# Performance work log

Measured on AMD Instinct MI355X. Metric: run time of the kernel, lower is better.

Reference implementation:

```python
import jax, jax.numpy as jnp
import numpy as np

N_NODES = 4096
N_EDGES = 32768
IN_FEAT = 256
OUT_FEAT = 128
HID = 64
IN_HEAD = 64
OUT_HEAD = 5
NEG_SLOPE = 0.2
EPS = 1e-16


def setup_inputs() -> dict:
    key = jax.random.key(0)
    ks = jax.random.split(key, 12)
    x = jax.random.normal(ks[0], (N_NODES, IN_FEAT), dtype=jnp.float32)
    src = jax.random.randint(ks[1], (N_EDGES,), 0, N_NODES)
    dst = jax.random.randint(ks[2], (N_EDGES,), 0, N_NODES)
    edge_index = jnp.stack([src, dst]).astype(jnp.int64)
    s1 = 1.0 / np.sqrt(IN_FEAT)
    s2 = 1.0 / np.sqrt(HID * IN_HEAD)
    W1 = jax.random.normal(ks[3], (IN_FEAT, IN_HEAD * HID), dtype=jnp.float32) * s1
    att_src1 = jax.random.normal(ks[4], (IN_HEAD, HID), dtype=jnp.float32) * 0.1
    att_dst1 = jax.random.normal(ks[5], (IN_HEAD, HID), dtype=jnp.float32) * 0.1
    b1 = jnp.zeros((IN_HEAD * HID,), dtype=jnp.float32)
    W2 = jax.random.normal(ks[6], (IN_HEAD * HID, OUT_HEAD * OUT_FEAT), dtype=jnp.float32) * s2
    att_src2 = jax.random.normal(ks[7], (OUT_HEAD, OUT_FEAT), dtype=jnp.float32) * 0.1
    att_dst2 = jax.random.normal(ks[8], (OUT_HEAD, OUT_FEAT), dtype=jnp.float32) * 0.1
    b2 = jnp.zeros((OUT_FEAT,), dtype=jnp.float32)
    return {"x": x, "edge_index": edge_index, "W1": W1, "att_src1": att_src1,
            "att_dst1": att_dst1, "b1": b1, "W2": W2, "att_src2": att_src2,
            "att_dst2": att_dst2, "b2": b2}


def _gat_conv(x, W, att_src, att_dst, bias, src, dst, heads, out_c, concat):
    # x: [N, F_in]; returns [N, heads*out_c] (concat) or [N, out_c] (mean)
    n = x.shape[0]
    h = (x @ W).reshape(n, heads, out_c)                       # [N,H,C]
    a_src = jnp.sum(h * att_src, axis=-1)                      # [N,H]
    a_dst = jnp.sum(h * att_dst, axis=-1)                      # [N,H]
    e = jax.nn.leaky_relu(a_src[src] + a_dst[dst], NEG_SLOPE)  # [E,H]
    # segment softmax over edges grouped by destination node (PyG softmax)
    m = jax.ops.segment_max(e, dst, num_segments=n)            # [N,H]
    ex = jnp.exp(e - m[dst])
    denom = jax.ops.segment_sum(ex, dst, num_segments=n)       # [N,H]
    alpha = ex / (denom[dst] + EPS)                            # [E,H]
    out = jax.ops.segment_sum(alpha[:, :, None] * h[src], dst, num_segments=n)  # [N,H,C]
    out = out.reshape(n, heads * out_c) if concat else out.mean(axis=1)
    return out + bias


def reference(x, edge_index, W1, att_src1, att_dst1, b1, W2, att_src2, att_dst2, b2):
    n = x.shape[0]
    # PyG GATConv default: add self loops
    loop = jnp.arange(n, dtype=edge_index.dtype)
    src = jnp.concatenate([edge_index[0], loop])
    dst = jnp.concatenate([edge_index[1], loop])
    # dropout layers are identity in eval mode
    h = _gat_conv(x, W1, att_src1, att_dst1, b1, src, dst, IN_HEAD, HID, True)
    h = jax.nn.elu(h)
    h = _gat_conv(h, W2, att_src2, att_dst2, b2, src, dst, OUT_HEAD, OUT_FEAT, False)
    s = jnp.mean(h, axis=0)
    return jnp.tanh(s)
```

## Files before the change

kernel.cpp:

```cpp
#include <hip/hip_runtime.h>
#include <hip/hip_bf16.h>

#define N_NODES 4096
#define NE      32768
#define E_TOT   (NE + N_NODES)
#define IN_FEAT 256
#define HID     64
#define IN_HEAD 64
#define F1      4096
#define OUT_HEAD 5
#define OUT_FEAT 128
#define F2      640
#define NEG_SLOPE 0.2f
#define EPS_A   1e-16f

typedef __bf16 bf16;
typedef bf16 bf16x8 __attribute__((ext_vector_type(8)));
typedef bf16 bf16x4 __attribute__((ext_vector_type(4)));
typedef float f32x4 __attribute__((ext_vector_type(4)));

__device__ inline void async_cp16(bf16* lds, const bf16* g) {
    __builtin_amdgcn_global_load_lds(
        (const __attribute__((address_space(1))) unsigned int*)g,
        (__attribute__((address_space(3))) unsigned int*)lds, 16, 0, 0);
}

template <typename TC>
__device__ __forceinline__ void gemm_body(
    const bf16* __restrict__ A, const bf16* __restrict__ BT, TC* __restrict__ Cz,
    int m0, int n0, int kbeg, int kchunk, int Ncols, int Kdim,
    bf16 (*As)[64], bf16 (*Bs)[64], int tid) {
    const int wave = tid >> 6, lane = tid & 63;
    const int quad = lane >> 4, lr = lane & 15;
    const int wm = (wave >> 1) * 64;
    const int wn = (wave & 1) * 64;
    const int srow = lane >> 3;
    const int scol = ((lane & 7) ^ srow) * 8;
    const int xk = lr & 7;

    f32x4 acc[4][4] = {};

    for (int kk = 0; kk < kchunk; kk += 64) {
        int k0 = kbeg + kk;
#pragma unroll
        for (int c = 0; c < 4; ++c) {
            int r = wave * 32 + c * 8;
            async_cp16(&As[r][0], A + (size_t)(m0 + r + srow) * Kdim + k0 + scol);
            async_cp16(&Bs[r][0], BT + (size_t)(n0 + r + srow) * Kdim + k0 + scol);
        }
        __syncthreads();

#pragma unroll
        for (int ks = 0; ks < 2; ++ks) {
            int ch = ((ks * 4 + quad) ^ xk) * 8;
            bf16x8 af[4], bfr[4];
#pragma unroll
            for (int mt = 0; mt < 4; ++mt)
                af[mt] = *(const bf16x8*)(&As[wm + mt * 16 + lr][ch]);
#pragma unroll
            for (int nt = 0; nt < 4; ++nt)
                bfr[nt] = *(const bf16x8*)(&Bs[wn + nt * 16 + lr][ch]);
#pragma unroll
            for (int mt = 0; mt < 4; ++mt)
#pragma unroll
                for (int nt = 0; nt < 4; ++nt)
                    acc[mt][nt] = __builtin_amdgcn_mfma_f32_16x16x32_bf16(
                        af[mt], bfr[nt], acc[mt][nt], 0, 0, 0);
        }
        __syncthreads();
    }

#pragma unroll
    for (int mt = 0; mt < 4; ++mt)
#pragma unroll
        for (int nt = 0; nt < 4; ++nt) {
            int row0 = m0 + wm + mt * 16 + quad * 4;
            int col = n0 + wn + nt * 16 + lr;
#pragma unroll
            for (int r = 0; r < 4; ++r)
                Cz[(size_t)(row0 + r) * Ncols + col] = (TC)acc[mt][nt][r];
        }
}

#define PB_H   144
#define PB_X   512
#define PB_W1  1024
#define PB_W2  2560
__global__ __launch_bounds__(256)
void phaseA_kernel(const int* __restrict__ edst, int* __restrict__ counts,
                   const float* __restrict__ x, bf16* __restrict__ xb,
                   const float* __restrict__ W1, bf16* __restrict__ W1T,
                   const float* __restrict__ W2, bf16* __restrict__ W2T,
                   const float* __restrict__ as1, const float* __restrict__ ad1,
                   bf16* __restrict__ w1s, bf16* __restrict__ w1d) {
    __shared__ float tile[32][33];
    int b0 = blockIdx.x, t = threadIdx.x;
    if (b0 < PB_H) {
        int e = b0 * 256 + t;
        if (e < E_TOT) {
            int d = (e < NE) ? edst[e] : (e - NE);
            atomicAdd(&counts[d], 1);
        }
        return;
    }
    int b = b0 - PB_H;
    if (b < PB_X) {
        int i = b * 256 + t;
        f32x4 a = *(const f32x4*)(x + (size_t)i * 8);
        f32x4 c = *(const f32x4*)(x + (size_t)i * 8 + 4);
        bf16x8 r;
        r[0] = (bf16)a[0]; r[1] = (bf16)a[1]; r[2] = (bf16)a[2]; r[3] = (bf16)a[3];
        r[4] = (bf16)c[0]; r[5] = (bf16)c[1]; r[6] = (bf16)c[2]; r[7] = (bf16)c[3];
        *(bf16x8*)(xb + (size_t)i * 8) = r;
    } else if (b < PB_X + PB_W1 + PB_W2) {
        const float* S; bf16* D; int R, C, gx, gy;
        if (b < PB_X + PB_W1) {
            int bb = b - PB_X;
            S = W1; D = W1T; R = IN_FEAT; C = F1;
            gx = bb % (F1 / 32); gy = bb / (F1 / 32);
        } else {
            int bb = b - PB_X - PB_W1;
            S = W2; D = W2T; R = F1; C = F2;
            gx = bb % (F2 / 32); gy = bb / (F2 / 32);
        }
        int tx = t & 31, ty = t >> 5;
        int c0 = gx * 32, r0 = gy * 32;
#pragma unroll
        for (int i = 0; i < 4; ++i)
            tile[ty + i * 8][tx] = S[(size_t)(r0 + ty + i * 8) * C + c0 + tx];
        __syncthreads();
#pragma unroll
        for (int i = 0; i < 4; ++i)
            D[(size_t)(c0 + ty + i * 8) * R + r0 + tx] = (bf16)tile[tx][ty + i * 8];
    } else {
        int id = (b - PB_X - PB_W1 - PB_W2) * 256 + t;
        int k = id >> 6, h = id & 63;
        const float* wrow = W1 + (size_t)k * F1 + h * HID;
        const float* a1 = as1 + h * HID;
        const float* a2 = ad1 + h * HID;
        float s = 0.f, d = 0.f;
#pragma unroll 8
        for (int c = 0; c < HID; ++c) {
            float w = wrow[c];
            s += w * a1[c];
            d += w * a2[c];
        }
        w1s[id] = (bf16)s;
        w1d[id] = (bf16)d;
    }
}

__global__ void scan_kernel(const int* __restrict__ counts,
                            int* __restrict__ row_start, int* __restrict__ cursor) {
    __shared__ int part[256];
    __shared__ int pre[257];
    int t = threadIdx.x;
    int base = t * 16;
    int local[16];
    int s = 0;
#pragma unroll
    for (int i = 0; i < 16; ++i) { local[i] = s; s += counts[base + i]; }
    part[t] = s;
    __syncthreads();
    if (t == 0) {
        int r = 0;
        for (int i = 0; i < 256; ++i) { pre[i] = r; r += part[i]; }
        pre[256] = r;
    }
    __syncthreads();
    int off = pre[t];
#pragma unroll
    for (int i = 0; i < 16; ++i) {
        int v = off + local[i];
        row_start[base + i] = v;
        cursor[base + i] = v;
    }
    if (t == 0) row_start[N_NODES] = pre[256];
}

#define PC_S   144
#define PC_G1  1024
__global__ __launch_bounds__(256)
void phaseC_kernel(const int* __restrict__ edst, int* cursor, int* __restrict__ elist,
                   const bf16* __restrict__ xb, const bf16* __restrict__ W1T,
                   bf16* __restrict__ H1,
                   const float* __restrict__ x,
                   const bf16* __restrict__ w1s, const bf16* __restrict__ w1d,
                   float* __restrict__ a_src, float* __restrict__ a_dst) {
    __shared__ bf16 As[128][64];
    __shared__ bf16 Bs[128][64];
    int b = blockIdx.x, t = threadIdx.x;
    if (b < PC_S) {
        int e = b * 256 + t;
        if (e < E_TOT) {
            int d = (e < NE) ? edst[e] : (e - NE);
            int slot = atomicAdd(&cursor[d], 1);
            elist[slot] = e;
        }
    } else if (b < PC_S + PC_G1) {
        int bid = b - PC_S;
        int xx = bid & 7, q = bid >> 3;
        int mb = xx * 4 + (q >> 5);
        int nb = q & 31;
        gemm_body<bf16>(xb, W1T, H1, mb * 128, nb * 128, 0, IN_FEAT,
                        F1, IN_FEAT, As, Bs, t);
    } else {
        int nblk = b - PC_S - PC_G1;
        int wave = t >> 6, lane = t & 63;
        int n = nblk * 4 + wave;
        const float* xr = x + (size_t)n * IN_FEAT;
        float s = 0.f, d = 0.f;
        for (int k0 = 0; k0 < IN_FEAT; k0 += 4) {
            f32x4 xv = *(const f32x4*)(xr + k0);
#pragma unroll
            for (int j = 0; j < 4; ++j) {
                float xs = xv[j];
                s += xs * (float)w1s[(k0 + j) * IN_HEAD + lane];
                d += xs * (float)w1d[(k0 + j) * IN_HEAD + lane];
            }
        }
        a_src[n * IN_HEAD + lane] = s;
        a_dst[n * IN_HEAD + lane] = d;
    }
}

__global__ __launch_bounds__(64)
void agg1_kernel(const int* __restrict__ es, const int* __restrict__ row_start,
                 const int* __restrict__ elist,
                 const float* __restrict__ a_src, const float* __restrict__ a_dst,
                 const bf16* __restrict__ H1, const float* __restrict__ b1,
                 bf16* __restrict__ h_elu) {
    int bid = blockIdx.x;
    int c = bid & 7;
    int d = bid >> 3;
    int lane = threadIdx.x;
    int gh = c * 8 + (lane >> 3);
    int sub = lane & 7;
    int beg = row_start[d], deg = row_start[d + 1] - beg;
    float adst = a_dst[d * IN_HEAD + gh];

    float m = -1e30f, den = 0.f;
    for (int i = sub; i < deg; i += 8) {
        int e = elist[beg + i];
        int s = (e < NE) ? es[e] : d;
        float l = a_src[s * IN_HEAD + gh] + adst;
        l = l > 0.f ? l : NEG_SLOPE * l;
        if (l > m) { den = den * __expf(m - l) + 1.f; m = l; }
        else den += __expf(l - m);
    }
#pragma unroll
    for (int o = 1; o <= 4; o <<= 1) {
        float mo = __shfl_xor(m, o);
        float dno = __shfl_xor(den, o);
        float mn = fmaxf(m, mo);
        den = den * __expf(m - mn) + dno * __expf(mo - mn);
        m = mn;
    }
    float dinv = 1.f / (den + EPS_A);

    int fbase = c * 512 + lane * 8;
    float acc[8] = {};
#pragma unroll 2
    for (int i = 0; i < deg; ++i) {
        int e = elist[beg + i];
        int s = (e < NE) ? es[e] : d;
        float l = a_src[s * IN_HEAD + gh] + adst;
        l = l > 0.f ? l : NEG_SLOPE * l;
        float alpha = __expf(l - m) * dinv;
        bf16x8 v = *(const bf16x8*)(H1 + (size_t)s * F1 + fbase);
#pragma unroll
        for (int j = 0; j < 8; ++j) acc[j] += alpha * (float)v[j];
    }

    bf16x8 o;
#pragma unroll
    for (int j = 0; j < 8; ++j) {
        float v = acc[j] + b1[fbase + j];
        o[j] = (bf16)(v > 0.f ? v : (__expf(v) - 1.f));
    }
    *(bf16x8*)(h_elu + (size_t)d * F1 + fbase) = o;
}

__global__ __launch_bounds__(256)
void gemm2_kernel(const bf16* __restrict__ A, const bf16* __restrict__ BT,
                  bf16* __restrict__ C) {
    __shared__ bf16 As[128][64];
    __shared__ bf16 Bs[128][64];
    int bid = blockIdx.x;
    int xx = bid & 7, q = bid >> 3;
    int gp = q / 5, nb = q - gp * 5;
    int g = gp * 8 + xx;
    int mb = g >> 2, zb = g & 3;
    const int kchunk = F1 / 4;
    gemm_body<bf16>(A, BT, C + (size_t)zb * N_NODES * F2,
                    mb * 128, nb * 128, zb * kchunk, kchunk,
                    F2, F1, As, Bs, threadIdx.x);
}

__global__ __launch_bounds__(192)
void fold2_kernel(const bf16* __restrict__ Hp,
                  const float* __restrict__ as2, const float* __restrict__ ad2,
                  float* __restrict__ H2,
                  float* __restrict__ a_src, float* __restrict__ a_dst) {
    int n = blockIdx.x, t = threadIdx.x;
    if (t >= 160) return;
    int h = t >> 5;
    f32x4 sum = {};
#pragma unroll
    for (int z = 0; z < 4; ++z) {
        bf16x4 v = *(const bf16x4*)(Hp + (size_t)z * N_NODES * F2 + (size_t)n * F2 + t * 4);
        sum[0] += (float)v[0]; sum[1] += (float)v[1];
        sum[2] += (float)v[2]; sum[3] += (float)v[3];
    }
    *(f32x4*)(H2 + (size_t)n * F2 + t * 4) = sum;
    f32x4 ws = *(const f32x4*)(as2 + t * 4);
    f32x4 wd = *(const f32x4*)(ad2 + t * 4);
    float s = sum[0] * ws[0] + sum[1] * ws[1] + sum[2] * ws[2] + sum[3] * ws[3];
    float d = sum[0] * wd[0] + sum[1] * wd[1] + sum[2] * wd[2] + sum[3] * wd[3];
#pragma unroll
    for (int o = 1; o <= 16; o <<= 1) {
        s += __shfl_xor(s, o);
        d += __shfl_xor(d, o);
    }
    if ((t & 31) == 0) {
        a_src[n * OUT_HEAD + h] = s;
        a_dst[n * OUT_HEAD + h] = d;
    }
}

__global__ void statsbeta2_kernel(const int* __restrict__ es,
                                  const int* __restrict__ row_start,
                                  const int* __restrict__ elist,
                                  const float* __restrict__ a_src,
                                  const float* __restrict__ a_dst,
                                  float* __restrict__ beta) {
    int id = blockIdx.x * 256 + threadIdx.x;
    if (id >= N_NODES * OUT_HEAD) return;
    int d = id / OUT_HEAD, h = id - d * OUT_HEAD;
    int beg = row_start[d], deg = row_start[d + 1] - beg;
    float adst = a_dst[id];
    float m = -1e30f, den = 0.f;
    for (int i = 0; i < deg; ++i) {
        int e = elist[beg + i];
        int s = (e < NE) ? es[e] : d;
        float l = a_src[s * OUT_HEAD + h] + adst;
        l = l > 0.f ? l : NEG_SLOPE * l;
        if (l > m) { den = den * __expf(m - l) + 1.f; m = l; }
        else den += __expf(l - m);
    }
    float dinv = 1.f / (den + EPS_A);
    for (int i = 0; i < deg; ++i) {
        int e = elist[beg + i];
        int s = (e < NE) ? es[e] : d;
        float l = a_src[s * OUT_HEAD + h] + adst;
        l = l > 0.f ? l : NEG_SLOPE * l;
        float alpha = __expf(l - m) * dinv;
        atomicAdd(&beta[s * OUT_HEAD + h], alpha);
    }
}

__global__ __launch_bounds__(256)
void wsum_kernel(const float* __restrict__ H2, const float* __restrict__ beta,
                 float* __restrict__ acc_out, int* __restrict__ done_ctr,
                 const float* __restrict__ b2, float* __restrict__ out) {
    __shared__ float buf[F2];
    __shared__ int lflag;
    int t = threadIdx.x;
    int n0 = blockIdx.x * 32;
    int h = t >> 5;
    float a0 = 0.f, a1 = 0.f, a2 = 0.f, a3 = 0.f;
    if (t < 160) {
        for (int i = 0; i < 32; ++i) {
            int s = n0 + i;
            float bh = beta[s * OUT_HEAD + h];
            f32x4 v = *(const f32x4*)(H2 + (size_t)s * F2 + t * 4);
            a0 += bh * v[0]; a1 += bh * v[1];
            a2 += bh * v[2]; a3 += bh * v[3];
        }
        buf[t * 4 + 0] = a0; buf[t * 4 + 1] = a1;
        buf[t * 4 + 2] = a2; buf[t * 4 + 3] = a3;
    }
    __syncthreads();
    if (t < OUT_FEAT) {
        float s = 0.f;
#pragma unroll
        for (int hh = 0; hh < OUT_HEAD; ++hh) s += buf[hh * OUT_FEAT + t];
        atomicAdd(&acc_out[(blockIdx.x & 7) * OUT_FEAT + t], s);
    }
    __threadfence();
    __syncthreads();
    if (t == 0) lflag = (atomicAdd(done_ctr, 1) == (N_NODES / 32) - 1);
    __syncthreads();
    if (lflag && t < OUT_FEAT) {
        float tot = 0.f;
#pragma unroll
        for (int k = 0; k < 8; ++k)
            tot += __hip_atomic_load(&acc_out[k * OUT_FEAT + t],
                                     __ATOMIC_RELAXED, __HIP_MEMORY_SCOPE_AGENT);
        out[t] = tanhf(tot * (1.f / (OUT_HEAD * (float)N_NODES)) + b2[t]);
    }
}

extern "C" void kernel_launch(void* const* d_in, const int* in_sizes, int n_in,
                              void* d_out, int out_size, void* d_ws, size_t ws_size,
                              hipStream_t stream) {
    const float* x        = (const float*)d_in[0];
    const int*   ei       = (const int*)d_in[1];
    const float* W1       = (const float*)d_in[2];
    const float* att_src1 = (const float*)d_in[3];
    const float* att_dst1 = (const float*)d_in[4];
    const float* b1       = (const float*)d_in[5];
    const float* W2       = (const float*)d_in[6];
    const float* att_src2 = (const float*)d_in[7];
    const float* att_dst2 = (const float*)d_in[8];
    const float* b2       = (const float*)d_in[9];
    float* out = (float*)d_out;

    const int* esrc = ei;
    const int* edst = ei + NE;

    char* p = (char*)d_ws;
    auto bump = [&](size_t bytes) {
        void* r = (void*)p;
        p += (bytes + 255) & ~(size_t)255;
        return r;
    };
    bf16*  H1     = (bf16*)bump((size_t)N_NODES * F1 * 2);
    bf16*  h_elu  = (bf16*)bump((size_t)N_NODES * F1 * 2);
    float* H2     = (float*)bump((size_t)N_NODES * F2 * 4);
    bf16*  xb     = (bf16*)bump((size_t)N_NODES * IN_FEAT * 2);
    bf16*  W1T    = (bf16*)bump((size_t)F1 * IN_FEAT * 2);
    bf16*  W2T    = (bf16*)bump((size_t)F2 * F1 * 2);
    bf16*  w1s    = (bf16*)bump((size_t)IN_FEAT * IN_HEAD * 2);
    bf16*  w1d    = (bf16*)bump((size_t)IN_FEAT * IN_HEAD * 2);
    float* a_src1 = (float*)bump((size_t)N_NODES * IN_HEAD * 4);
    float* a_dst1 = (float*)bump((size_t)N_NODES * IN_HEAD * 4);
    float* a_src2 = (float*)bump((size_t)N_NODES * OUT_HEAD * 4);
    float* a_dst2 = (float*)bump((size_t)N_NODES * OUT_HEAD * 4);
    int*   row_start = (int*)bump((N_NODES + 1) * 4);
    int*   cursor = (int*)bump(N_NODES * 4);
    int*   elist  = (int*)bump(E_TOT * 4);
    size_t zbytes = N_NODES * 4 + N_NODES * OUT_HEAD * 4 + 8 * OUT_FEAT * 4 + 256;
    int*   counts = (int*)bump(zbytes);
    float* beta    = (float*)((char*)counts + N_NODES * 4);
    float* acc_out = beta + N_NODES * OUT_HEAD;
    int*   done_ctr = (int*)(acc_out + 8 * OUT_FEAT);
    bf16* Hp = H1;

    hipMemsetAsync(counts, 0, zbytes, stream);

    phaseA_kernel<<<PB_H + PB_X + PB_W1 + PB_W2 + 64, 256, 0, stream>>>(
        edst, counts, x, xb, W1, W1T, W2, W2T, att_src1, att_dst1, w1s, w1d);
    scan_kernel<<<1, 256, 0, stream>>>(counts, row_start, cursor);
    phaseC_kernel<<<PC_S + PC_G1 + N_NODES / 4, 256, 0, stream>>>(
        edst, cursor, elist, xb, W1T, H1, x, w1s, w1d, a_src1, a_dst1);
    agg1_kernel<<<N_NODES * 8, 64, 0, stream>>>(
        esrc, row_start, elist, a_src1, a_dst1, H1, b1, h_elu);
    gemm2_kernel<<<640, 256, 0, stream>>>(h_elu, W2T, Hp);
    fold2_kernel<<<N_NODES, 192, 0, stream>>>(
        Hp, att_src2, att_dst2, H2, a_src2, a_dst2);
    statsbeta2_kernel<<<(N_NODES * OUT_HEAD + 255) / 256, 256, 0, stream>>>(
        esrc, row_start, elist, a_src2, a_dst2, beta);
    wsum_kernel<<<N_NODES / 32, 256, 0, stream>>>(
        H2, beta, acc_out, done_ctr, b2, out);
}
```

Measured before the change: 256.4 us.

## Fuse all GAT phases into one cooperative persistent kernel with grid syncs

Replaces the eight separate kernel launches and memset with a single cooperative persistent kernel that walks through each phase in grid-stride loops, separated by grid.sync(). It also changes the second GEMM to a split-K over 8 chunks with a reduction in the fold step, and splits the layer-2 softmax stats and the beta scatter into per-node and per-edge passes. This aims to remove launch overhead and tail gaps between phases, at the cost of capped occupancy (768 blocks, launch bounds of 3), the cost of each grid barrier, and extra split-K partial traffic.

```diff
diff --git a/kernel.cpp b/kernel.cpp
--- a/kernel.cpp
+++ b/kernel.cpp
@@ -1,5 +1,8 @@
 #include <hip/hip_runtime.h>
 #include <hip/hip_bf16.h>
+#include <hip/hip_cooperative_groups.h>
+
+namespace cg = cooperative_groups;
 
 #define N_NODES 4096
 #define NE      32768
@@ -13,6 +16,7 @@
 #define F2      640
 #define NEG_SLOPE 0.2f
 #define EPS_A   1e-16f
+#define ZSPLIT  8
 
 typedef __bf16 bf16;
 typedef bf16 bf16x8 __attribute__((ext_vector_type(8)));
@@ -49,7 +53,6 @@
             async_cp16(&Bs[r][0], BT + (size_t)(n0 + r + srow) * Kdim + k0 + scol);
         }
         __syncthreads();
-
 #pragma unroll
         for (int ks = 0; ks < 2; ++ks) {
             int ch = ((ks * 4 + quad) ^ xk) * 8;
@@ -81,343 +84,332 @@
                 Cz[(size_t)(row0 + r) * Ncols + col] = (TC)acc[mt][nt][r];
         }
 }
+
+struct MegaArgs {
+    const int* esrc; const int* edst;
+    const float *x, *W1, *as1, *ad1, *b1, *W2, *as2, *ad2, *b2;
+    float* out;
+    bf16 *H1, *h_elu, *Hp, *xb, *W1T, *W2T, *w1s, *w1d;
+    float *H2, *a_src1, *a_dst1, *a_src2, *a_dst2, *m2, *dinv2;
+    int *row_start, *cursor;
+    int *elist;
+    int *counts;
+    float *beta, *acc_out;
+};
 
 #define PB_H   144
 #define PB_X   512
 #define PB_W1  1024
 #define PB_W2  2560
-__global__ __launch_bounds__(256)
-void phaseA_kernel(const int* __restrict__ edst, int* __restrict__ counts,
-                   const float* __restrict__ x, bf16* __restrict__ xb,
-                   const float* __restrict__ W1, bf16* __restrict__ W1T,
-                   const float* __restrict__ W2, bf16* __restrict__ W2T,
-                   const float* __restrict__ as1, const float* __restrict__ ad1,
-                   bf16* __restrict__ w1s, bf16* __restrict__ w1d) {
-    __shared__ float tile[32][33];
-    int b0 = blockIdx.x, t = threadIdx.x;
-    if (b0 < PB_H) {
-        int e = b0 * 256 + t;
-        if (e < E_TOT) {
-            int d = (e < NE) ? edst[e] : (e - NE);
-            atomicAdd(&counts[d], 1);
-        }
-        return;
-    }
-    int b = b0 - PB_H;
-    if (b < PB_X) {
-        int i = b * 256 + t;
-        f32x4 a = *(const f32x4*)(x + (size_t)i * 8);
-        f32x4 c = *(const f32x4*)(x + (size_t)i * 8 + 4);
-        bf16x8 r;
-        r[0] = (bf16)a[0]; r[1] = (bf16)a[1]; r[2] = (bf16)a[2]; r[3] = (bf16)a[3];
-        r[4] = (bf16)c[0]; r[5] = (bf16)c[1]; r[6] = (bf16)c[2]; r[7] = (bf16)c[3];
-        *(bf16x8*)(xb + (size_t)i * 8) = r;
-    } else if (b < PB_X + PB_W1 + PB_W2) {
-        const float* S; bf16* D; int R, C, gx, gy;
-        if (b < PB_X + PB_W1) {
-            int bb = b - PB_X;
-            S = W1; D = W1T; R = IN_FEAT; C = F1;
-            gx = bb % (F1 / 32); gy = bb / (F1 / 32);
+#define P1_TOT (PB_H + PB_X + PB_W1 + PB_W2 + 64)
+#define P3_G1  1024
+#define P3_SC  144
+#define P3_TOT (P3_G1 + P3_SC + 1024)
+#define ZWORDS (N_NODES + N_NODES * OUT_HEAD + 8 * OUT_FEAT)
+
+__global__ __launch_bounds__(256, 3)
+void mega_kernel(MegaArgs a) {
+    cg::grid_group grid = cg::this_grid();
+    const int b = blockIdx.x, t = threadIdx.x;
+    const int gs = gridDim.x;
+    const int wave = t >> 6, lane = t & 63;
+
+    __shared__ alignas(16) char lds[32768];
+    bf16 (*As)[64] = reinterpret_cast<bf16(*)[64]>(lds);
+    bf16 (*Bs)[64] = reinterpret_cast<bf16(*)[64]>(lds + 16384);
+    float (*tile)[33] = reinterpret_cast<float(*)[33]>(lds);
+    int* part = reinterpret_cast<int*>(lds);
+    int* pre  = reinterpret_cast<int*>(lds + 1024);
+    float* buf = reinterpret_cast<float*>(lds);
+
+    for (int i = b * 256 + t; i < ZWORDS; i += gs * 256) a.counts[i] = 0;
+    grid.sync();
+
+    for (int u = b; u < P1_TOT; u += gs) {
+        if (u < PB_H) {
+            int e = u * 256 + t;
+            if (e < E_TOT) {
+                int d = (e < NE) ? a.edst[e] : (e - NE);
+                atomicAdd(&a.counts[d], 1);
+            }
+        } else if (u < PB_H + PB_X) {
+            int i = (u - PB_H) * 256 + t;
+            f32x4 v0 = *(const f32x4*)(a.x + (size_t)i * 8);
+            f32x4 v1 = *(const f32x4*)(a.x + (size_t)i * 8 + 4);
+            bf16x8 r;
+            r[0] = (bf16)v0[0]; r[1] = (bf16)v0[1]; r[2] = (bf16)v0[2]; r[3] = (bf16)v0[3];
+            r[4] = (bf16)v1[0]; r[5] = (bf16)v1[1]; r[6] = (bf16)v1[2]; r[7] = (bf16)v1[3];
+            *(bf16x8*)(a.xb + (size_t)i * 8) = r;
+        } else if (u < PB_H + PB_X + PB_W1 + PB_W2) {
+            const float* S; bf16* D; int R, C, gx, gy;
+            int bb = u - PB_H - PB_X;
+            if (bb < PB_W1) {
+                S = a.W1; D = a.W1T; R = IN_FEAT; C = F1;
+                gx = bb % (F1 / 32); gy = bb / (F1 / 32);
+            } else {
+                bb -= PB_W1;
+                S = a.W2; D = a.W2T; R = F1; C = F2;
+                gx = bb % (F2 / 32); gy = bb / (F2 / 32);
+            }
+            int tx = t & 31, ty = t >> 5;
+            int c0 = gx * 32, r0 = gy * 32;
+            __syncthreads();
+#pragma unroll
+            for (int i = 0; i < 4; ++i)
+                tile[ty + i * 8][tx] = S[(size_t)(r0 + ty + i * 8) * C + c0 + tx];
+            __syncthreads();
+#pragma unroll
+            for (int i = 0; i < 4; ++i)
+                D[(size_t)(c0 + ty + i * 8) * R + r0 + tx] = (bf16)tile[tx][ty + i * 8];
         } else {
-            int bb = b - PB_X - PB_W1;
-            S = W2; D = W2T; R = F1; C = F2;
-            gx = bb % (F2 / 32); gy = bb / (F2 / 32);
-        }
-        int tx = t & 31, ty = t >> 5;
-        int c0 = gx * 32, r0 = gy * 32;
-#pragma unroll
-        for (int i = 0; i < 4; ++i)
-            tile[ty + i * 8][tx] = S[(size_t)(r0 + ty + i * 8) * C + c0 + tx];
-        __syncthreads();
-#pragma unroll
-        for (int i = 0; i < 4; ++i)
-            D[(size_t)(c0 + ty + i * 8) * R + r0 + tx] = (bf16)tile[tx][ty + i * 8];
-    } else {
-        int id = (b - PB_X - PB_W1 - PB_W2) * 256 + t;
-        int k = id >> 6, h = id & 63;
-        const float* wrow = W1 + (size_t)k * F1 + h * HID;
-        const float* a1 = as1 + h * HID;
-        const float* a2 = ad1 + h * HID;
-        float s = 0.f, d = 0.f;
+            int id = (u - PB_H - PB_X - PB_W1 - PB_W2) * 256 + t;
+            int k = id >> 6, h = id & 63;
+            const float* wrow = a.W1 + (size_t)k * F1 + h * HID;
+            const float* a1 = a.as1 + h * HID;
+            const float* a2 = a.ad1 + h * HID;
+            float s = 0.f, d = 0.f;
 #pragma unroll 8
-        for (int c = 0; c < HID; ++c) {
-            float w = wrow[c];
-            s += w * a1[c];
-            d += w * a2[c];
-        }
-        w1s[id] = (bf16)s;
-        w1d[id] = (bf16)d;
-    }
-}
-
-__global__ void scan_kernel(const int* __restrict__ counts,
-                            int* __restrict__ row_start, int* __restrict__ cursor) {
-    __shared__ int part[256];
-    __shared__ int pre[257];
-    int t = threadIdx.x;
-    int base = t * 16;
-    int local[16];
-    int s = 0;
-#pragma unroll
-    for (int i = 0; i < 16; ++i) { local[i] = s; s += counts[base + i]; }
-    part[t] = s;
-    __syncthreads();
-    if (t == 0) {
-        int r = 0;
-        for (int i = 0; i < 256; ++i) { pre[i] = r; r += part[i]; }
-        pre[256] = r;
-    }
-    __syncthreads();
-    int off = pre[t];
-#pragma unroll
-    for (int i = 0; i < 16; ++i) {
-        int v = off + local[i];
-        row_start[base + i] = v;
-        cursor[base + i] = v;
-    }
-    if (t == 0) row_start[N_NODES] = pre[256];
-}
-
-#define PC_S   144
-#define PC_G1  1024
-__global__ __launch_bounds__(256)
-void phaseC_kernel(const int* __restrict__ edst, int* cursor, int* __restrict__ elist,
-                   const bf16* __restrict__ xb, const bf16* __restrict__ W1T,
-                   bf16* __restrict__ H1,
-                   const float* __restrict__ x,
-                   const bf16* __restrict__ w1s, const bf16* __restrict__ w1d,
-                   float* __restrict__ a_src, float* __restrict__ a_dst) {
-    __shared__ bf16 As[128][64];
-    __shared__ bf16 Bs[128][64];
-    int b = blockIdx.x, t = threadIdx.x;
-    if (b < PC_S) {
-        int e = b * 256 + t;
-        if (e < E_TOT) {
-            int d = (e < NE) ? edst[e] : (e - NE);
-            int slot = atomicAdd(&cursor[d], 1);
-            elist[slot] = e;
-        }
-    } else if (b < PC_S + PC_G1) {
-        int bid = b - PC_S;
-        int xx = bid & 7, q = bid >> 3;
-        int mb = xx * 4 + (q >> 5);
-        int nb = q & 31;
-        gemm_body<bf16>(xb, W1T, H1, mb * 128, nb * 128, 0, IN_FEAT,
-                        F1, IN_FEAT, As, Bs, t);
-    } else {
-        int nblk = b - PC_S - PC_G1;
-        int wave = t >> 6, lane = t & 63;
-        int n = nblk * 4 + wave;
-        const float* xr = x + (size_t)n * IN_FEAT;
-        float s = 0.f, d = 0.f;
-        for (int k0 = 0; k0 < IN_FEAT; k0 += 4) {
-            f32x4 xv = *(const f32x4*)(xr + k0);
-#pragma unroll
-            for (int j = 0; j < 4; ++j) {
-                float xs = xv[j];
-                s += xs * (float)w1s[(k0 + j) * IN_HEAD + lane];
-                d += xs * (float)w1d[(k0 + j) * IN_HEAD + lane];
-            }
-        }
-        a_src[n * IN_HEAD + lane] = s;
-        a_dst[n * IN_HEAD + lane] = d;
-    }
-}
-
-__global__ __launch_bounds__(64)
-void agg1_kernel(const int* __restrict__ es, const int* __restrict__ row_start,
-                 const int* __restrict__ elist,
-                 const float* __restrict__ a_src, const float* __restrict__ a_dst,
-                 const bf16* __restrict__ H1, const float* __restrict__ b1,
-                 bf16* __restrict__ h_elu) {
-    int bid = blockIdx.x;
-    int c = bid & 7;
-    int d = bid >> 3;
-    int lane = threadIdx.x;
-    int gh = c * 8 + (lane >> 3);
-    int sub = lane & 7;
-    int beg = row_start[d], deg = row_start[d + 1] - beg;
-    float adst = a_dst[d * IN_HEAD + gh];
-
-    float m = -1e30f, den = 0.f;
-    for (int i = sub; i < deg; i += 8) {
-        int e = elist[beg + i];
-        int s = (e < NE) ? es[e] : d;
-        float l = a_src[s * IN_HEAD + gh] + adst;
+            for (int c = 0; c < HID; ++c) {
+                float w = wrow[c];
+                s += w * a1[c];
+                d += w * a2[c];
+            }
+            a.w1s[id] = (bf16)s;
+            a.w1d[id] = (bf16)d;
+        }
+    }
+    grid.sync();
+
+    if (b == 0) {
+        int base = t * 16;
+        int local[16];
+        int s = 0;
+#pragma unroll
+        for (int i = 0; i < 16; ++i) { local[i] = s; s += a.counts[base + i]; }
+        part[t] = s;
+        __syncthreads();
+        if (t == 0) {
+            int r = 0;
+            for (int i = 0; i < 256; ++i) { pre[i] = r; r += part[i]; }
+            pre[256] = r;
+        }
+        __syncthreads();
+        int off = pre[t];
+#pragma unroll
+        for (int i = 0; i < 16; ++i) {
+            int v = off + local[i];
+            a.row_start[base + i] = v;
+            a.cursor[base + i] = v;
+        }
+        if (t == 0) a.row_start[N_NODES] = pre[256];
+    }
+    grid.sync();
+
+    for (int u = b; u < P3_TOT; u += gs) {
+        if (u < P3_G1) {
+            int xx = u & 7, q = u >> 3;
+            int mb = xx * 4 + (q >> 5);
+            int nb = q & 31;
+            gemm_body<bf16>(a.xb, a.W1T, a.H1, mb * 128, nb * 128, 0, IN_FEAT,
+                            F1, IN_FEAT, As, Bs, t);
+        } else if (u < P3_G1 + P3_SC) {
+            int e = (u - P3_G1) * 256 + t;
+            if (e < E_TOT) {
+                int d = (e < NE) ? a.edst[e] : (e - NE);
+                int slot = atomicAdd(&a.cursor[d], 1);
+                a.elist[slot] = e;
+            }
+        } else {
+            int n = (u - P3_G1 - P3_SC) * 4 + wave;
+            const float* xr = a.x + (size_t)n * IN_FEAT;
+            float s = 0.f, d = 0.f;
+            for (int k0 = 0; k0 < IN_FEAT; k0 += 4) {
+                f32x4 xv = *(const f32x4*)(xr + k0);
+#pragma unroll
+                for (int j = 0; j < 4; ++j) {
+                    float xs = xv[j];
+                    s += xs * (float)a.w1s[(k0 + j) * IN_HEAD + lane];
+                    d += xs * (float)a.w1d[(k0 + j) * IN_HEAD + lane];
+                }
+            }
+            a.a_src1[n * IN_HEAD + lane] = s;
+            a.a_dst1[n * IN_HEAD + lane] = d;
+        }
+    }
+    grid.sync();
+
+    {
+        int c = b & 7;
+        int wps = (gs >> 3) * 4;
+        int wIdx = (b >> 3) * 4 + wave;
+        int gh = c * 8 + (lane >> 3);
+        int sub = lane & 7;
+        int fbase = c * 512 + lane * 8;
+        for (int d = wIdx; d < N_NODES; d += wps) {
+            int beg = a.row_start[d], deg = a.row_start[d + 1] - beg;
+            float adst = a.a_dst1[d * IN_HEAD + gh];
+            float m = -1e30f, den = 0.f;
+            for (int i = sub; i < deg; i += 8) {
+                int e = a.elist[beg + i];
+                int s = (e < NE) ? a.esrc[e] : d;
+                float l = a.a_src1[s * IN_HEAD + gh] + adst;
+                l = l > 0.f ? l : NEG_SLOPE * l;
+                if (l > m) { den = den * __expf(m - l) + 1.f; m = l; }
+                else den += __expf(l - m);
+            }
+#pragma unroll
+            for (int o = 1; o <= 4; o <<= 1) {
+                float mo = __shfl_xor(m, o);
+                float dno = __shfl_xor(den, o);
+                float mn = fmaxf(m, mo);
+                den = den * __expf(m - mn) + dno * __expf(mo - mn);
+                m = mn;
+            }
+            float dinv = 1.f / (den + EPS_A);
+
+            float acc[8] = {};
+#pragma unroll 2
+            for (int i = 0; i < deg; ++i) {
+                int e = a.elist[beg + i];
+                int s = (e < NE) ? a.esrc[e] : d;
+                float l = a.a_src1[s * IN_HEAD + gh] + adst;
+                l = l > 0.f ? l : NEG_SLOPE * l;
+                float alpha = __expf(l - m) * dinv;
+                bf16x8 v = *(const bf16x8*)(a.H1 + (size_t)s * F1 + fbase);
+#pragma unroll
+                for (int j = 0; j < 8; ++j) acc[j] += alpha * (float)v[j];
+            }
+            bf16x8 o;
+#pragma unroll
+            for (int j = 0; j < 8; ++j) {
+                float v = acc[j] + a.b1[fbase + j];
+                o[j] = (bf16)(v > 0.f ? v : (__expf(v) - 1.f));
+            }
+            *(bf16x8*)(a.h_elu + (size_t)d * F1 + fbase) = o;
+        }
+    }
+    grid.sync();
+
+    for (int u = b; u < ZSPLIT * 160; u += gs) {
+        int xx = u & 7, q = u >> 3;
+        int gp = q / 5, nb = q - gp * 5;
+        int mb = gp, zb = xx;
+        const int kchunk = F1 / ZSPLIT;
+        gemm_body<bf16>(a.h_elu, a.W2T, a.Hp + (size_t)zb * N_NODES * F2,
+                        mb * 128, nb * 128, zb * kchunk, kchunk,
+                        F2, F1, As, Bs, t);
+    }
+    grid.sync();
+
+    for (int n = b; n < N_NODES; n += gs) {
+        if (t < 160) {
+            int h = t >> 5;
+            f32x4 sum = {};
+#pragma unroll
+            for (int z = 0; z < ZSPLIT; ++z) {
+                bf16x4 v = *(const bf16x4*)(a.Hp + (size_t)z * N_NODES * F2 +
+                                            (size_t)n * F2 + t * 4);
+                sum[0] += (float)v[0]; sum[1] += (float)v[1];
+                sum[2] += (float)v[2]; sum[3] += (float)v[3];
+            }
+            *(f32x4*)(a.H2 + (size_t)n * F2 + t * 4) = sum;
+            f32x4 ws = *(const f32x4*)(a.as2 + t * 4);
+            f32x4 wd = *(const f32x4*)(a.ad2 + t * 4);
+            float s = sum[0]*ws[0] + sum[1]*ws[1] + sum[2]*ws[2] + sum[3]*ws[3];
+            float d = sum[0]*wd[0] + sum[1]*wd[1] + sum[2]*wd[2] + sum[3]*wd[3];
+#pragma unroll
+            for (int o = 1; o <= 16; o <<= 1) {
+                s += __shfl_xor(s, o);
+                d += __shfl_xor(d, o);
+            }
+            if ((t & 31) == 0) {
+                a.a_src2[n * OUT_HEAD + h] = s;
+                a.a_dst2[n * OUT_HEAD + h] = d;
+            }
+        }
+    }
+    grid.sync();
+
+    for (int id = b * 256 + t; id < N_NODES * OUT_HEAD; id += gs * 256) {
+        int d = id / OUT_HEAD, h = id - d * OUT_HEAD;
+        int beg = a.row_start[d], deg = a.row_start[d + 1] - beg;
+        float adst = a.a_dst2[id];
+        float m = -1e30f, den = 0.f;
+        for (int i = 0; i < deg; ++i) {
+            int e = a.elist[beg + i];
+            int s = (e < NE) ? a.esrc[e] : d;
+            float l = a.a_src2[s * OUT_HEAD + h] + adst;
+            l = l > 0.f ? l : NEG_SLOPE * l;
+            if (l > m) { den = den * __expf(m - l) + 1.f; m = l; }
+            else den += __expf(l - m);
+        }
+        a.m2[id] = m;
+        a.dinv2[id] = 1.f / (den + EPS_A);
+    }
+    grid.sync();
+
+    for (int id = b * 256 + t; id < E_TOT * OUT_HEAD; id += gs * 256) {
+        int e = id / OUT_HEAD, h = id - e * OUT_HEAD;
+        int s = (e < NE) ? a.esrc[e] : (e - NE);
+        int d = (e < NE) ? a.edst[e] : (e - NE);
+        float l = a.a_src2[s * OUT_HEAD + h] + a.a_dst2[d * OUT_HEAD + h];
         l = l > 0.f ? l : NEG_SLOPE * l;
-        if (l > m) { den = den * __expf(m - l) + 1.f; m = l; }
-        else den += __expf(l - m);
-    }
-#pragma unroll
-    for (int o = 1; o <= 4; o <<= 1) {
-        float mo = __shfl_xor(m, o);
-        float dno = __shfl_xor(den, o);
-        float mn = fmaxf(m, mo);
-        den = den * __expf(m - mn) + dno * __expf(mo - mn);
-        m = mn;
-    }
-    float dinv = 1.f / (den + EPS_A);
-
-    int fbase = c * 512 + lane * 8;
-    float acc[8] = {};
-#pragma unroll 2
-    for (int i = 0; i < deg; ++i) {
-        int e = elist[beg + i];
-        int s = (e < NE) ? es[e] : d;
-        float l = a_src[s * IN_HEAD + gh] + adst;
-        l = l > 0.f ? l : NEG_SLOPE * l;
-        float alpha = __expf(l - m) * dinv;
-        bf16x8 v = *(const bf16x8*)(H1 + (size_t)s * F1 + fbase);
-#pragma unroll
-        for (int j = 0; j < 8; ++j) acc[j] += alpha * (float)v[j];
-    }
-
-    bf16x8 o;
-#pragma unroll
-    for (int j = 0; j < 8; ++j) {
-        float v = acc[j] + b1[fbase + j];
-        o[j] = (bf16)(v > 0.f ? v : (__expf(v) - 1.f));
-    }
-    *(bf16x8*)(h_elu + (size_t)d * F1 + fbase) = o;
-}
-
-__global__ __launch_bounds__(256)
-void gemm2_kernel(const bf16* __restrict__ A, const bf16* __restrict__ BT,
-                  bf16* __restrict__ C) {
-    __shared__ bf16 As[128][64];
-    __shared__ bf16 Bs[128][64];
-    int bid = blockIdx.x;
-    int xx = bid & 7, q = bid >> 3;
-    int gp = q / 5, nb = q - gp * 5;
-    int g = gp * 8 + xx;
-    int mb = g >> 2, zb = g & 3;
-    const int kchunk = F1 / 4;
-    gemm_body<bf16>(A, BT, C + (size_t)zb * N_NODES * F2,
-                    mb * 128, nb * 128, zb * kchunk, kchunk,
-                    F2, F1, As, Bs, threadIdx.x);
-}
-
-__global__ __launch_bounds__(192)
-void fold2_kernel(const bf16* __restrict__ Hp,
-                  const float* __restrict__ as2, const float* __restrict__ ad2,
-                  float* __restrict__ H2,
-                  float* __restrict__ a_src, float* __restrict__ a_dst) {
-    int n = blockIdx.x, t = threadIdx.x;
-    if (t >= 160) return;
-    int h = t >> 5;
-    f32x4 sum = {};
-#pragma unroll
-    for (int z = 0; z < 4; ++z) {
-        bf16x4 v = *(const bf16x4*)(Hp + (size_t)z * N_NODES * F2 + (size_t)n * F2 + t * 4);
-        sum[0] += (float)v[0]; sum[1] += (float)v[1];
-        sum[2] += (float)v[2]; sum[3] += (float)v[3];
-    }
-    *(f32x4*)(H2 + (size_t)n * F2 + t * 4) = sum;
-    f32x4 ws = *(const f32x4*)(as2 + t * 4);
-    f32x4 wd = *(const f32x4*)(ad2 + t * 4);
-    float s = sum[0] * ws[0] + sum[1] * ws[1] + sum[2] * ws[2] + sum[3] * ws[3];
-    float d = sum[0] * wd[0] + sum[1] * wd[1] + sum[2] * wd[2] + sum[3] * wd[3];
-#pragma unroll
-    for (int o = 1; o <= 16; o <<= 1) {
-        s += __shfl_xor(s, o);
-        d += __shfl_xor(d, o);
-    }
-    if ((t & 31) == 0) {
-        a_src[n * OUT_HEAD + h] = s;
-        a_dst[n * OUT_HEAD + h] = d;
-    }
-}
-
-__global__ void statsbeta2_kernel(const int* __restrict__ es,
-                                  const int* __restrict__ row_start,
-                                  const int* __restrict__ elist,
-                                  const float* __restrict__ a_src,
-                                  const float* __restrict__ a_dst,
-                                  float* __restrict__ beta) {
-    int id = blockIdx.x * 256 + threadIdx.x;
-    if (id >= N_NODES * OUT_HEAD) return;
-    int d = id / OUT_HEAD, h = id - d * OUT_HEAD;
-    int beg = row_start[d], deg = row_start[d + 1] - beg;
-    float adst = a_dst[id];
-    float m = -1e30f, den = 0.f;
-    for (int i = 0; i < deg; ++i) {
-        int e = elist[beg + i];
-        int s = (e < NE) ? es[e] : d;
-        float l = a_src[s * OUT_HEAD + h] + adst;
-        l = l > 0.f ? l : NEG_SLOPE * l;
-        if (l > m) { den = den * __expf(m - l) + 1.f; m = l; }
-        else den += __expf(l - m);
-    }
-    float dinv = 1.f / (den + EPS_A);
-    for (int i = 0; i < deg; ++i) {
-        int e = elist[beg + i];
-        int s = (e < NE) ? es[e] : d;
-        float l = a_src[s * OUT_HEAD + h] + adst;
-        l = l > 0.f ? l : NEG_SLOPE * l;
-        float alpha = __expf(l - m) * dinv;
-        atomicAdd(&beta[s * OUT_HEAD + h], alpha);
-    }
-}
-
-__global__ __launch_bounds__(256)
-void wsum_kernel(const float* __restrict__ H2, const float* __restrict__ beta,
-                 float* __restrict__ acc_out, int* __restrict__ done_ctr,
-                 const float* __restrict__ b2, float* __restrict__ out) {
-    __shared__ float buf[F2];
-    __shared__ int lflag;
-    int t = threadIdx.x;
-    int n0 = blockIdx.x * 32;
-    int h = t >> 5;
-    float a0 = 0.f, a1 = 0.f, a2 = 0.f, a3 = 0.f;
-    if (t < 160) {
-        for (int i = 0; i < 32; ++i) {
-            int s = n0 + i;
-            float bh = beta[s * OUT_HEAD + h];
-            f32x4 v = *(const f32x4*)(H2 + (size_t)s * F2 + t * 4);
-            a0 += bh * v[0]; a1 += bh * v[1];
-            a2 += bh * v[2]; a3 += bh * v[3];
-        }
-        buf[t * 4 + 0] = a0; buf[t * 4 + 1] = a1;
-        buf[t * 4 + 2] = a2; buf[t * 4 + 3] = a3;
-    }
-    __syncthreads();
-    if (t < OUT_FEAT) {
-        float s = 0.f;
-#pragma unroll
-        for (int hh = 0; hh < OUT_HEAD; ++hh) s += buf[hh * OUT_FEAT + t];
-        atomicAdd(&acc_out[(blockIdx.x & 7) * OUT_FEAT + t], s);
-    }
-    __threadfence();
-    __syncthreads();
-    if (t == 0) lflag = (atomicAdd(done_ctr, 1) == (N_NODES / 32) - 1);
-    __syncthreads();
-    if (lflag && t < OUT_FEAT) {
+        float alpha = __expf(l - a.m2[d * OUT_HEAD + h]) * a.dinv2[d * OUT_HEAD + h];
+        atomicAdd(&a.beta[s * OUT_HEAD + h], alpha);
+    }
+    grid.sync();
+
+    for (int u = b; u < N_NODES / 32; u += gs) {
+        int n0 = u * 32;
+        int h = t >> 5;
+        float a0 = 0.f, a1 = 0.f, a2 = 0.f, a3 = 0.f;
+        __syncthreads();
+        if (t < 160) {
+            for (int i = 0; i < 32; ++i) {
+                int s = n0 + i;
+                float bh = a.beta[s * OUT_HEAD + h];
+                f32x4 v = *(const f32x4*)(a.H2 + (size_t)s * F2 + t * 4);
+                a0 += bh * v[0]; a1 += bh * v[1];
+                a2 += bh * v[2]; a3 += bh * v[3];
+            }
+            buf[t * 4 + 0] = a0; buf[t * 4 + 1] = a1;
+            buf[t * 4 + 2] = a2; buf[t * 4 + 3] = a3;
+        }
+        __syncthreads();
+        if (t < OUT_FEAT) {
+            float s = 0.f;
+#pragma unroll
+            for (int hh = 0; hh < OUT_HEAD; ++hh) s += buf[hh * OUT_FEAT + t];
+            atomicAdd(&a.acc_out[(u & 7) * OUT_FEAT + t], s);
+        }
+    }
+    grid.sync();
+
+    if (b == 0 && t < OUT_FEAT) {
         float tot = 0.f;
 #pragma unroll
-        for (int k = 0; k < 8; ++k)
-            tot += __hip_atomic_load(&acc_out[k * OUT_FEAT + t],
-                                     __ATOMIC_RELAXED, __HIP_MEMORY_SCOPE_AGENT);
-        out[t] = tanhf(tot * (1.f / (OUT_HEAD * (float)N_NODES)) + b2[t]);
+        for (int k = 0; k < 8; ++k) tot += a.acc_out[k * OUT_FEAT + t];
+        a.out[t] = tanhf(tot * (1.f / (OUT_HEAD * (float)N_NODES)) + a.b2[t]);
     }
 }
 
 extern "C" void kernel_launch(void* const* d_in, const int* in_sizes, int n_in,
                               void* d_out, int out_size, void* d_ws, size_t ws_size,
                               hipStream_t stream) {
-    const float* x        = (const float*)d_in[0];
-    const int*   ei       = (const int*)d_in[1];
-    const float* W1       = (const float*)d_in[2];
-    const float* att_src1 = (const float*)d_in[3];
-    const float* att_dst1 = (const float*)d_in[4];
-    const float* b1       = (const float*)d_in[5];
-    const float* W2       = (const float*)d_in[6];
-    const float* att_src2 = (const float*)d_in[7];
-    const float* att_dst2 = (const float*)d_in[8];
-    const float* b2       = (const float*)d_in[9];
-    float* out = (float*)d_out;
-
-    const int* esrc = ei;
-    const int* edst = ei + NE;
+    MegaArgs a;
+    a.x   = (const float*)d_in[0];
+    const int* ei = (const int*)d_in[1];
+    a.W1  = (const float*)d_in[2];
+    a.as1 = (const float*)d_in[3];
+    a.ad1 = (const float*)d_in[4];
+    a.b1  = (const float*)d_in[5];
+    a.W2  = (const float*)d_in[6];
+    a.as2 = (const float*)d_in[7];
+    a.ad2 = (const float*)d_in[8];
+    a.b2  = (const float*)d_in[9];
+    a.out = (float*)d_out;
+    a.esrc = ei;
+    a.edst = ei + NE;
 
     char* p = (char*)d_ws;
     auto bump = [&](size_t bytes) {
@@ -425,42 +417,36 @@
         p += (bytes + 255) & ~(size_t)255;
         return r;
     };
-    bf16*  H1     = (bf16*)bump((size_t)N_NODES * F1 * 2);
-    bf16*  h_elu  = (bf16*)bump((size_t)N_NODES * F1 * 2);
-    float* H2     = (float*)bump((size_t)N_NODES * F2 * 4);
-    bf16*  xb     = (bf16*)bump((size_t)N_NODES * IN_FEAT * 2);
-    bf16*  W1T    = (bf16*)bump((size_t)F1 * IN_FEAT * 2);
-    bf16*  W2T    = (bf16*)bump((size_t)F2 * F1 * 2);
-    bf16*  w1s    = (bf16*)bump((size_t)IN_FEAT * IN_HEAD * 2);
-    bf16*  w1d    = (bf16*)bump((size_t)IN_FEAT * IN_HEAD * 2);
-    float* a_src1 = (float*)bump((size_t)N_NODES * IN_HEAD * 4);
-    float* a_dst1 = (float*)bump((size_t)N_NODES * IN_HEAD * 4);
-    float* a_src2 = (float*)bump((size_t)N_NODES * OUT_HEAD * 4);
-    float* a_dst2 = (float*)bump((size_t)N_NODES * OUT_HEAD * 4);
-    int*   row_start = (int*)bump((N_NODES + 1) * 4);
-    int*   cursor = (int*)bump(N_NODES * 4);
-    int*   elist  = (int*)bump(E_TOT * 4);
-    size_t zbytes = N_NODES * 4 + N_NODES * OUT_HEAD * 4 + 8 * OUT_FEAT * 4 + 256;
-    int*   counts = (int*)bump(zbytes);
-    float* beta    = (float*)((char*)counts + N_NODES * 4);
-    float* acc_out = beta + N_NODES * OUT_HEAD;
-    int*   done_ctr = (int*)(acc_out + 8 * OUT_FEAT);
-    bf16* Hp = H1;
-
-    hipMemsetAsync(counts, 0, zbytes, stream);
-
-    phaseA_kernel<<<PB_H + PB_X + PB_W1 + PB_W2 + 64, 256, 0, stream>>>(
-        edst, counts, x, xb, W1, W1T, W2, W2T, att_src1, att_dst1, w1s, w1d);
-    scan_kernel<<<1, 256, 0, stream>>>(counts, row_start, cursor);
-    phaseC_kernel<<<PC_S + PC_G1 + N_NODES / 4, 256, 0, stream>>>(
-        edst, cursor, elist, xb, W1T, H1, x, w1s, w1d, a_src1, a_dst1);
-    agg1_kernel<<<N_NODES * 8, 64, 0, stream>>>(
-        esrc, row_start, elist, a_src1, a_dst1, H1, b1, h_elu);
-    gemm2_kernel<<<640, 256, 0, stream>>>(h_elu, W2T, Hp);
-    fold2_kernel<<<N_NODES, 192, 0, stream>>>(
-        Hp, att_src2, att_dst2, H2, a_src2, a_dst2);
-    statsbeta2_kernel<<<(N_NODES * OUT_HEAD + 255) / 256, 256, 0, stream>>>(
-        esrc, row_start, elist, a_src2, a_dst2, beta);
-    wsum_kernel<<<N_NODES / 32, 256, 0, stream>>>(
-        H2, beta, acc_out, done_ctr, b2, out);
+    a.H1     = (bf16*)bump((size_t)N_NODES * F1 * 2);
+    a.h_elu  = (bf16*)bump((size_t)N_NODES * F1 * 2);
+    a.H2     = (float*)bump((size_t)N_NODES * F2 * 4);
+    a.Hp     = (bf16*)bump((size_t)ZSPLIT * N_NODES * F2 * 2);
+    a.xb     = (bf16*)bump((size_t)N_NODES * IN_FEAT * 2);
+    a.W1T    = (bf16*)bump((size_t)F1 * IN_FEAT * 2);
+    a.W2T    = (bf16*)bump((size_t)F2 * F1 * 2);
+    a.w1s    = (bf16*)bump((size_t)IN_FEAT * IN_HEAD * 2);
+    a.w1d    = (bf16*)bump((size_t)IN_FEAT * IN_HEAD * 2);
+    a.a_src1 = (float*)bump((size_t)N_NODES * IN_HEAD * 4);
+    a.a_dst1 = (float*)bump((size_t)N_NODES * IN_HEAD * 4);
+    a.a_src2 = (float*)bump((size_t)N_NODES * OUT_HEAD * 4);
+    a.a_dst2 = (float*)bump((size_t)N_NODES * OUT_HEAD * 4);
+    a.m2     = (float*)bump((size_t)N_NODES * OUT_HEAD * 4);
+    a.dinv2  = (float*)bump((size_t)N_NODES * OUT_HEAD * 4);
+    a.row_start = (int*)bump((N_NODES + 1) * 4);
+    a.cursor = (int*)bump(N_NODES * 4);
+    a.elist  = (int*)bump(E_TOT * 4);
+    a.counts = (int*)bump((size_t)ZWORDS * 4);
+    a.beta    = (float*)(a.counts + N_NODES);
+    a.acc_out = a.beta + N_NODES * OUT_HEAD;
+
+    int maxB = 2;
+    hipOccupancyMaxActiveBlocksPerMultiprocessor(&maxB, mega_kernel, 256, 0);
+    int grid = maxB * 256;
+    if (grid > 768) grid = 768;
+    grid = (grid / 8) * 8;
+    if (grid < 8) grid = 8;
+
+    void* kargs[] = { &a };
+    hipLaunchCooperativeKernel((const void*)mega_kernel, dim3(grid), dim3(256),
+                               kargs, 0, stream);
 }
```

New measurement: 714.3 us. +178.6%, slower.
